# Performance work log

Measured on AMD Instinct MI355X. Metric: run time of the kernel, lower is better.

Reference implementation:

```python
import jax, jax.numpy as jnp
from jax import lax
import numpy as np

WINDOW_SIZE = 11
SIGMA = 1.5
C1 = 0.01 ** 2
C2 = 0.03 ** 2


def _make_window(window_size, channel):
    x = np.arange(window_size) - window_size // 2
    g = np.exp(-(x ** 2) / (2.0 * SIGMA ** 2))
    g = g / g.sum()
    w3 = g[:, None, None] * g[None, :, None] * g[None, None, :]  # [k,k,k]
    w = np.broadcast_to(w3, (channel, 1, window_size, window_size, window_size))
    return jnp.asarray(w.copy(), dtype=jnp.float32)


def setup_inputs() -> dict:
    key = jax.random.key(0)
    k1, k2 = jax.random.split(key)
    shape = (4, 1, 160, 160, 160)
    img1 = jax.random.uniform(k1, shape, dtype=jnp.float32)
    img2 = jax.random.uniform(k2, shape, dtype=jnp.float32)
    window = _make_window(WINDOW_SIZE, shape[1])
    return {"img1": img1, "img2": img2, "window": window}


def _depthwise_conv3d(x, window):
    c = window.shape[0]
    k = window.shape[-1]
    pad = k // 2
    return lax.conv_general_dilated(
        x, window,
        window_strides=(1, 1, 1),
        padding=[(pad, pad)] * 3,
        dimension_numbers=("NCDHW", "OIDHW", "NCDHW"),
        feature_group_count=c,
    )


def reference(img1, img2, window):
    b = img1.shape[0]
    # One conv call over all five window statistics (stacked along batch).
    stacked = jnp.concatenate(
        [img1, img2, img1 * img1, img2 * img2, img1 * img2], axis=0)
    conv = _depthwise_conv3d(stacked, window)
    mu1, mu2, e11, e22, e12 = (conv[i * b:(i + 1) * b] for i in range(5))
    mu1_sq = mu1 * mu1
    mu2_sq = mu2 * mu2
    mu1_mu2 = mu1 * mu2
    sigma1_sq = e11 - mu1_sq
    sigma2_sq = e22 - mu2_sq
    sigma12 = e12 - mu1_mu2
    ssim_map = ((2 * mu1_mu2 + C1) * (2 * sigma12 + C2)) / (
        (mu1_sq + mu2_sq + C1) * (sigma1_sq + sigma2_sq + C2))
    return ssim_map.mean()  # size_average=True
```

## Files before the change

kernel.cpp:

```cpp
#include <hip/hip_runtime.h>
#include <math.h>
#include <type_traits>

typedef float f2 __attribute__((ext_vector_type(2)));
typedef float f4 __attribute__((ext_vector_type(4)));

#define DD 160
#define HH 160
#define WW 160
#define BB 4
#define KK 11
#define RAD 5
#define TH 16
#define TW 16
#define DCH 32
#define NPLANES (DCH + 2 * RAD)
#define NDCH (DD / DCH)
#define HALO_H (TH + 2 * RAD)
#define TS 16
#define STAT (HALO_H * TS)

struct GaussP { float gg[32]; };

__global__ __launch_bounds__(128, 2)
void ssim3d_kernel(const float* __restrict__ img1,
                   const float* __restrict__ img2,
                   float* __restrict__ out, GaussP gp)
{
    __shared__ float tmpA[5 * STAT];
    __shared__ float tmpB[5 * STAT];
    __shared__ float wsum[2];

    const int tid = threadIdx.x;
    const int xc = tid & 7;
    const int ty = tid >> 3;
    const int p1r = tid >> 2;
    const int p1q = tid & 3;

    const int blk = blockIdx.x;
    const int bw = blk % 10;
    const int bh = (blk / 10) % 10;
    const int bd = (blk / 100) % NDCH;
    const int bb = blk / (100 * NDCH);

    const int oh0 = bh * TH, ow0 = bw * TW, od0 = bd * DCH;
    const float* base1 = img1 + (size_t)bb * DD * HH * WW;
    const float* base2 = img2 + (size_t)bb * DD * HH * WW;

    f2 a1[KK], a2[KK], a11[KK], a22[KK], a12[KK];
#pragma unroll
    for (int i = 0; i < KK; ++i) { a1[i]=0.f; a2[i]=0.f; a11[i]=0.f; a22[i]=0.f; a12[i]=0.f; }

    f2 lsum = 0.f;

    const int gh = oh0 - RAD + p1r;
    const bool p1act = (p1r < HALO_H);
    const bool rowok = p1act && ((unsigned)gh < (unsigned)HH);
    const int gc0 = ow0 + 4 * p1q - 8;
    const size_t rowoff = (size_t)((unsigned)gh < (unsigned)HH ? gh : 0) * WW;

    f4 pa[5], pb[5];
#pragma unroll
    for (int j = 0; j < 5; ++j) { pa[j] = (f4)0.f; pb[j] = (f4)0.f; }

    float* twr = tmpA;
    float* trd = tmpB;

    {
        const int dn = od0 - RAD;
        if (p1act && (unsigned)dn < (unsigned)DD) {
            const size_t pbv = (size_t)dn * (HH * WW) + rowoff;
#pragma unroll
            for (int j = 0; j < 5; ++j) {
                const int gc = gc0 + 4 * j;
                f4 za = (f4)0.f, zb = (f4)0.f;
                if (rowok && gc >= 0 && gc <= WW - 4) {
                    za = *(const f4*)(base1 + pbv + gc);
                    zb = *(const f4*)(base2 + pbv + gc);
                }
                pa[j] = za; pb[j] = zb;
            }
        }
    }

    int pcbase = 0;
    auto body = [&](auto uc) {
        constexpr int U = decltype(uc)::value;
        const int p = pcbase + U;
        const int d = od0 - RAD + p;
        const bool dval = (p < NPLANES) && ((unsigned)d < (unsigned)DD);

        if (dval && p1act) {
            f2 q0[5], q1[5];
#pragma unroll
            for (int st = 0; st < 5; ++st) { q0[st] = 0.f; q1[st] = 0.f; }
#pragma unroll
            for (int j = 0; j < 5; ++j) {
#pragma unroll
                for (int ii = 0; ii < 4; ++ii) {
                    const int i = 4 * j + ii;
                    if (i < 3 || i > 16) continue;
                    const float av = pa[j][ii], bv = pb[j][ii];
                    const float aa = av * av, bb2 = bv * bv, ab = av * bv;
                    const f2 w01 = { gp.gg[2*(i-1)], gp.gg[2*(i-1)+1] };
                    const f2 w23 = { gp.gg[2*(i-3)], gp.gg[2*(i-3)+1] };
                    q0[0] += w01 * av;   q1[0] += w23 * av;
                    q0[1] += w01 * bv;   q1[1] += w23 * bv;
                    q0[2] += w01 * aa;   q1[2] += w23 * aa;
                    q0[3] += w01 * bb2;  q1[3] += w23 * bb2;
                    q0[4] += w01 * ab;   q1[4] += w23 * ab;
                }
            }
            float* tw = twr + p1r * TS + 4 * p1q;
#pragma unroll
            for (int st = 0; st < 5; ++st) {
                f4 v;
                v[0] = q0[st][0]; v[1] = q0[st][1];
                v[2] = q1[st][0]; v[3] = q1[st][1];
                *(f4*)(tw + st * STAT) = v;
            }
        }

        {
            const int pn = p + 1;
            const int dn = od0 - RAD + pn;
            if (p1act && (pn < NPLANES) && ((unsigned)dn < (unsigned)DD)) {
                const size_t pbv = (size_t)dn * (HH * WW) + rowoff;
#pragma unroll
                for (int j = 0; j < 5; ++j) {
                    const int gc = gc0 + 4 * j;
                    f4 za = (f4)0.f, zb = (f4)0.f;
                    if (rowok && gc >= 0 && gc <= WW - 4) {
                        za = *(const f4*)(base1 + pbv + gc);
                        zb = *(const f4*)(base2 + pbv + gc);
                    }
                    pa[j] = za; pb[j] = zb;
                }
            }
        }

        if (dval) {
            asm volatile("s_waitcnt lgkmcnt(0)\n\ts_barrier" ::: "memory");
            f2 P1 = 0.f, P2 = 0.f, P11 = 0.f, P22 = 0.f, P12 = 0.f;
            const float* tb = twr + (ty * TS + 2 * xc);
#pragma unroll
            for (int k = 0; k < KK; ++k) {
                const float w = gp.gg[2 * (k + 2)];
                const int o = k * TS;
                P1  += w * *(const f2*)(tb + 0*STAT + o);
                P2  += w * *(const f2*)(tb + 1*STAT + o);
                P11 += w * *(const f2*)(tb + 2*STAT + o);
                P22 += w * *(const f2*)(tb + 3*STAT + o);
                P12 += w * *(const f2*)(tb + 4*STAT + o);
            }
#pragma unroll
            for (int t = 0; t < KK; ++t) {
                constexpr int base = U + 22;
                const int s = (base - t) % 11;
                const float w = gp.gg[2 * (t + 2)];
                a1[s]  += w * P1;
                a2[s]  += w * P2;
                a11[s] += w * P11;
                a22[s] += w * P22;
                a12[s] += w * P12;
            }
        }

        constexpr int e = (U + 1) % 11;
        if (p >= 2 * RAD && p < NPLANES) {
            f2 mu1 = a1[e], mu2 = a2[e];
            f2 m11 = mu1 * mu1, m22 = mu2 * mu2, m12 = mu1 * mu2;
            f2 sg1 = a11[e] - m11, sg2 = a22[e] - m22, sg12 = a12[e] - m12;
            const float C1c = 0.0001f, C2c = 0.0009f;
            f2 num = (2.f * m12 + C1c) * (2.f * sg12 + C2c);
            f2 den = (m11 + m22 + C1c) * (sg1 + sg2 + C2c);
            lsum += num / den;
        }
        a1[e] = 0.f; a2[e] = 0.f; a11[e] = 0.f; a22[e] = 0.f; a12[e] = 0.f;

        float* t = twr; twr = trd; trd = t;
    };

    for (pcbase = 0; pcbase < 44; pcbase += 11) {
        body(std::integral_constant<int, 0>{});
        body(std::integral_constant<int, 1>{});
        body(std::integral_constant<int, 2>{});
        body(std::integral_constant<int, 3>{});
        body(std::integral_constant<int, 4>{});
        body(std::integral_constant<int, 5>{});
        body(std::integral_constant<int, 6>{});
        body(std::integral_constant<int, 7>{});
        body(std::integral_constant<int, 8>{});
        body(std::integral_constant<int, 9>{});
        body(std::integral_constant<int, 10>{});
    }

    float v = lsum.x + lsum.y;
#pragma unroll
    for (int off = 32; off > 0; off >>= 1)
        v += __shfl_down(v, off, 64);
    if ((tid & 63) == 0) wsum[tid >> 6] = v;
    __syncthreads();
    if (tid == 0) {
        const float inv_n = 1.0f / ((float)BB * DD * HH * WW);
        atomicAdd(out, (wsum[0] + wsum[1]) * inv_n);
    }
}

extern "C" void kernel_launch(void* const* d_in, const int* in_sizes, int n_in,
                              void* d_out, int out_size, void* d_ws, size_t ws_size,
                              hipStream_t stream) {
    const float* img1 = (const float*)d_in[0];
    const float* img2 = (const float*)d_in[1];
    float* out = (float*)d_out;

    double gd[KK], sum = 0.0;
    for (int i = 0; i < KK; ++i) {
        double x = (double)(i - KK / 2);
        gd[i] = exp(-(x * x) / (2.0 * 1.5 * 1.5));
        sum += gd[i];
    }
    float gf[KK];
    for (int i = 0; i < KK; ++i) gf[i] = (float)(gd[i] / sum);

    GaussP gp;
    for (int x = 0; x < 16; ++x) {
        const int j0 = x - 2, j1 = x - 3;
        gp.gg[2 * x]     = (j0 >= 0 && j0 < KK) ? gf[j0] : 0.0f;
        gp.gg[2 * x + 1] = (j1 >= 0 && j1 < KK) ? gf[j1] : 0.0f;
    }

    hipMemsetAsync(d_out, 0, sizeof(float), stream);

    dim3 grid(10 * 10 * NDCH * BB);
    dim3 block(128);
    hipLaunchKernelGGL(ssim3d_kernel, grid, block, 0, stream,
                       img1, img2, out, gp);
}
```

Before: 336.3 us.

## Process two depth planes per barrier with quad-buffered shared staging

The depth loop now handles two planes per iteration, staging both planes' horizontally filtered statistics into a four-slot shared buffer so only one barrier is needed per pair of planes. Two register prefetch sets keep two planes of global loads in flight. Phase-1 tasks are remapped so each wavefront uses 52 of its 64 lanes instead of leaving the last wave mostly idle. This halves barrier count and deepens the load pipeline, at the cost of more shared memory and more registers, which may hurt occupancy at two blocks per CU.

New measurement: 454.5 us. 35.2% more time.

```diff
diff --git a/kernel.cpp b/kernel.cpp
--- a/kernel.cpp
+++ b/kernel.cpp
@@ -22,20 +22,24 @@
 
 struct GaussP { float gg[32]; };
 
+template <int N> using ic = std::integral_constant<int, N>;
+
 __global__ __launch_bounds__(128, 2)
 void ssim3d_kernel(const float* __restrict__ img1,
                    const float* __restrict__ img2,
                    float* __restrict__ out, GaussP gp)
 {
-    __shared__ float tmpA[5 * STAT];
-    __shared__ float tmpB[5 * STAT];
+    __shared__ float tmp[4][5 * STAT];
     __shared__ float wsum[2];
 
     const int tid = threadIdx.x;
     const int xc = tid & 7;
     const int ty = tid >> 3;
-    const int p1r = tid >> 2;
-    const int p1q = tid & 3;
+    const int lane = tid & 63;
+    const int task = lane + (tid >> 6) * 52;
+    const bool p1act = lane < 52;
+    const int p1r = task >> 2;
+    const int p1q = task & 3;
 
     const int blk = blockIdx.x;
     const int bw = blk % 10;
@@ -54,21 +58,17 @@
     f2 lsum = 0.f;
 
     const int gh = oh0 - RAD + p1r;
-    const bool p1act = (p1r < HALO_H);
     const bool rowok = p1act && ((unsigned)gh < (unsigned)HH);
     const int gc0 = ow0 + 4 * p1q - 8;
     const size_t rowoff = (size_t)((unsigned)gh < (unsigned)HH ? gh : 0) * WW;
 
-    f4 pa[5], pb[5];
-#pragma unroll
-    for (int j = 0; j < 5; ++j) { pa[j] = (f4)0.f; pb[j] = (f4)0.f; }
-
-    float* twr = tmpA;
-    float* trd = tmpB;
-
-    {
-        const int dn = od0 - RAD;
-        if (p1act && (unsigned)dn < (unsigned)DD) {
+    f4 paA[5], pbA[5], paB[5], pbB[5];
+#pragma unroll
+    for (int j = 0; j < 5; ++j) { paA[j]=(f4)0.f; pbA[j]=(f4)0.f; paB[j]=(f4)0.f; pbB[j]=(f4)0.f; }
+
+    auto prefetch = [&](f4* pa, f4* pb, int pn) {
+        const int dn = od0 - RAD + pn;
+        if (p1act && (pn < NPLANES) && ((unsigned)dn < (unsigned)DD)) {
             const size_t pbv = (size_t)dn * (HH * WW) + rowoff;
 #pragma unroll
             for (int j = 0; j < 5; ++j) {
@@ -81,92 +81,70 @@
                 pa[j] = za; pb[j] = zb;
             }
         }
-    }
-
-    int pcbase = 0;
-    auto body = [&](auto uc) {
-        constexpr int U = decltype(uc)::value;
-        const int p = pcbase + U;
-        const int d = od0 - RAD + p;
-        const bool dval = (p < NPLANES) && ((unsigned)d < (unsigned)DD);
-
-        if (dval && p1act) {
-            f2 q0[5], q1[5];
-#pragma unroll
-            for (int st = 0; st < 5; ++st) { q0[st] = 0.f; q1[st] = 0.f; }
-#pragma unroll
-            for (int j = 0; j < 5; ++j) {
-#pragma unroll
-                for (int ii = 0; ii < 4; ++ii) {
-                    const int i = 4 * j + ii;
-                    if (i < 3 || i > 16) continue;
-                    const float av = pa[j][ii], bv = pb[j][ii];
-                    const float aa = av * av, bb2 = bv * bv, ab = av * bv;
-                    const f2 w01 = { gp.gg[2*(i-1)], gp.gg[2*(i-1)+1] };
-                    const f2 w23 = { gp.gg[2*(i-3)], gp.gg[2*(i-3)+1] };
-                    q0[0] += w01 * av;   q1[0] += w23 * av;
-                    q0[1] += w01 * bv;   q1[1] += w23 * bv;
-                    q0[2] += w01 * aa;   q1[2] += w23 * aa;
-                    q0[3] += w01 * bb2;  q1[3] += w23 * bb2;
-                    q0[4] += w01 * ab;   q1[4] += w23 * ab;
-                }
+    };
+
+    auto phase1 = [&](const f4* pa, const f4* pb, int p) {
+        if (!p1act) return;
+        f2 q0[5], q1[5];
+#pragma unroll
+        for (int st = 0; st < 5; ++st) { q0[st] = 0.f; q1[st] = 0.f; }
+#pragma unroll
+        for (int j = 0; j < 5; ++j) {
+#pragma unroll
+            for (int ii = 0; ii < 4; ++ii) {
+                const int i = 4 * j + ii;
+                if (i < 3 || i > 16) continue;
+                const float av = pa[j][ii], bv = pb[j][ii];
+                const float aa = av * av, bb2 = bv * bv, ab = av * bv;
+                const f2 w01 = { gp.gg[2*(i-1)], gp.gg[2*(i-1)+1] };
+                const f2 w23 = { gp.gg[2*(i-3)], gp.gg[2*(i-3)+1] };
+                q0[0] += w01 * av;   q1[0] += w23 * av;
+                q0[1] += w01 * bv;   q1[1] += w23 * bv;
+                q0[2] += w01 * aa;   q1[2] += w23 * aa;
+                q0[3] += w01 * bb2;  q1[3] += w23 * bb2;
+                q0[4] += w01 * ab;   q1[4] += w23 * ab;
             }
-            float* tw = twr + p1r * TS + 4 * p1q;
-#pragma unroll
-            for (int st = 0; st < 5; ++st) {
-                f4 v;
-                v[0] = q0[st][0]; v[1] = q0[st][1];
-                v[2] = q1[st][0]; v[3] = q1[st][1];
-                *(f4*)(tw + st * STAT) = v;
-            }
-        }
-
-        {
-            const int pn = p + 1;
-            const int dn = od0 - RAD + pn;
-            if (p1act && (pn < NPLANES) && ((unsigned)dn < (unsigned)DD)) {
-                const size_t pbv = (size_t)dn * (HH * WW) + rowoff;
-#pragma unroll
-                for (int j = 0; j < 5; ++j) {
-                    const int gc = gc0 + 4 * j;
-                    f4 za = (f4)0.f, zb = (f4)0.f;
-                    if (rowok && gc >= 0 && gc <= WW - 4) {
-                        za = *(const f4*)(base1 + pbv + gc);
-                        zb = *(const f4*)(base2 + pbv + gc);
-                    }
-                    pa[j] = za; pb[j] = zb;
-                }
-            }
-        }
-
-        if (dval) {
-            asm volatile("s_waitcnt lgkmcnt(0)\n\ts_barrier" ::: "memory");
-            f2 P1 = 0.f, P2 = 0.f, P11 = 0.f, P22 = 0.f, P12 = 0.f;
-            const float* tb = twr + (ty * TS + 2 * xc);
-#pragma unroll
-            for (int k = 0; k < KK; ++k) {
-                const float w = gp.gg[2 * (k + 2)];
-                const int o = k * TS;
-                P1  += w * *(const f2*)(tb + 0*STAT + o);
-                P2  += w * *(const f2*)(tb + 1*STAT + o);
-                P11 += w * *(const f2*)(tb + 2*STAT + o);
-                P22 += w * *(const f2*)(tb + 3*STAT + o);
-                P12 += w * *(const f2*)(tb + 4*STAT + o);
-            }
-#pragma unroll
-            for (int t = 0; t < KK; ++t) {
-                constexpr int base = U + 22;
-                const int s = (base - t) % 11;
-                const float w = gp.gg[2 * (t + 2)];
-                a1[s]  += w * P1;
-                a2[s]  += w * P2;
-                a11[s] += w * P11;
-                a22[s] += w * P22;
-                a12[s] += w * P12;
-            }
-        }
-
-        constexpr int e = (U + 1) % 11;
+        }
+        float* tw = tmp[p & 3] + p1r * TS + 4 * p1q;
+#pragma unroll
+        for (int st = 0; st < 5; ++st) {
+            f4 v;
+            v[0] = q0[st][0]; v[1] = q0[st][1];
+            v[2] = q1[st][0]; v[3] = q1[st][1];
+            *(f4*)(tw + st * STAT) = v;
+        }
+    };
+
+    auto phase2 = [&](auto ucU, int p) {
+        constexpr int UU = decltype(ucU)::value;
+        f2 P1 = 0.f, P2 = 0.f, P11 = 0.f, P22 = 0.f, P12 = 0.f;
+        const float* tb = tmp[p & 3] + (ty * TS + 2 * xc);
+#pragma unroll
+        for (int k = 0; k < KK; ++k) {
+            const float w = gp.gg[2 * (k + 2)];
+            const int o = k * TS;
+            P1  += w * *(const f2*)(tb + 0*STAT + o);
+            P2  += w * *(const f2*)(tb + 1*STAT + o);
+            P11 += w * *(const f2*)(tb + 2*STAT + o);
+            P22 += w * *(const f2*)(tb + 3*STAT + o);
+            P12 += w * *(const f2*)(tb + 4*STAT + o);
+        }
+#pragma unroll
+        for (int t = 0; t < KK; ++t) {
+            constexpr int base = UU + 22;
+            const int s = (base - t) % 11;
+            const float w = gp.gg[2 * (t + 2)];
+            a1[s]  += w * P1;
+            a2[s]  += w * P2;
+            a11[s] += w * P11;
+            a22[s] += w * P22;
+            a12[s] += w * P12;
+        }
+    };
+
+    auto emitp = [&](auto ucU, int p) {
+        constexpr int UU = decltype(ucU)::value;
+        constexpr int e = (UU + 1) % 11;
         if (p >= 2 * RAD && p < NPLANES) {
             f2 mu1 = a1[e], mu2 = a2[e];
             f2 m11 = mu1 * mu1, m22 = mu2 * mu2, m12 = mu1 * mu2;
@@ -177,22 +155,47 @@
             lsum += num / den;
         }
         a1[e] = 0.f; a2[e] = 0.f; a11[e] = 0.f; a22[e] = 0.f; a12[e] = 0.f;
-
-        float* t = twr; twr = trd; trd = t;
-    };
-
-    for (pcbase = 0; pcbase < 44; pcbase += 11) {
-        body(std::integral_constant<int, 0>{});
-        body(std::integral_constant<int, 1>{});
-        body(std::integral_constant<int, 2>{});
-        body(std::integral_constant<int, 3>{});
-        body(std::integral_constant<int, 4>{});
-        body(std::integral_constant<int, 5>{});
-        body(std::integral_constant<int, 6>{});
-        body(std::integral_constant<int, 7>{});
-        body(std::integral_constant<int, 8>{});
-        body(std::integral_constant<int, 9>{});
-        body(std::integral_constant<int, 10>{});
+    };
+
+    prefetch(paA, pbA, 0);
+    prefetch(paB, pbB, 1);
+
+    int pcbase = 0;
+    auto iter = [&](auto ucv) {
+        constexpr int V = decltype(ucv)::value;
+        const int p0 = pcbase + 2 * V;
+        const int p1 = p0 + 1;
+        const int d0 = od0 - RAD + p0;
+        const bool dval0 = (p0 < NPLANES) && ((unsigned)d0 < (unsigned)DD);
+        const bool dval1 = (p1 < NPLANES) && ((unsigned)(d0 + 1) < (unsigned)DD);
+
+        if (dval0) phase1(paA, pbA, p0);
+        prefetch(paA, pbA, p0 + 2);
+        if (dval1) phase1(paB, pbB, p1);
+        prefetch(paB, pbB, p1 + 2);
+
+        if (dval0 || dval1) {
+            asm volatile("s_waitcnt lgkmcnt(0)\n\ts_barrier" ::: "memory");
+        }
+
+        if (dval0) phase2(ic<(2 * V) % 11>{}, p0);
+        emitp(ic<(2 * V) % 11>{}, p0);
+        if (dval1) phase2(ic<(2 * V + 1) % 11>{}, p1);
+        emitp(ic<(2 * V + 1) % 11>{}, p1);
+    };
+
+    for (pcbase = 0; pcbase < 44; pcbase += 22) {
+        iter(ic<0>{});
+        iter(ic<1>{});
+        iter(ic<2>{});
+        iter(ic<3>{});
+        iter(ic<4>{});
+        iter(ic<5>{});
+        iter(ic<6>{});
+        iter(ic<7>{});
+        iter(ic<8>{});
+        iter(ic<9>{});
+        iter(ic<10>{});
     }
 
     float v = lsum.x + lsum.y;
```

## Shrink tile to one wavefront per block and drop the LDS barrier

Applied to the files above, without the earlier changes.

Halves the tile width so each block is a single 64-thread wavefront, doubles the grid, and replaces the s_barrier with just an lgkmcnt wait. The shared-memory stride is padded from 16 to 20, and the cross-wave final reduction is removed. The aim is to remove workgroup barrier stalls and gain scheduling flexibility. In exchange, the relative halo overhead in W grows (8-wide outputs need 18 input columns), so each output costs more global loads and more first-pass convolution work.

Measured after the change: 437.9 us. 1.3x slower.

```diff
diff --git a/kernel.cpp b/kernel.cpp
--- a/kernel.cpp
+++ b/kernel.cpp
@@ -12,36 +12,37 @@
 #define KK 11
 #define RAD 5
 #define TH 16
-#define TW 16
+#define TW 8
 #define DCH 32
 #define NPLANES (DCH + 2 * RAD)
 #define NDCH (DD / DCH)
 #define HALO_H (TH + 2 * RAD)
-#define TS 16
+#define TS 20
 #define STAT (HALO_H * TS)
 
 struct GaussP { float gg[32]; };
 
-__global__ __launch_bounds__(128, 2)
+template <int N> using ic = std::integral_constant<int, N>;
+
+__global__ __launch_bounds__(64, 2)
 void ssim3d_kernel(const float* __restrict__ img1,
                    const float* __restrict__ img2,
                    float* __restrict__ out, GaussP gp)
 {
-    __shared__ float tmpA[5 * STAT];
-    __shared__ float tmpB[5 * STAT];
-    __shared__ float wsum[2];
+    __shared__ float tmp[2][5 * STAT];
 
     const int tid = threadIdx.x;
-    const int xc = tid & 7;
-    const int ty = tid >> 3;
-    const int p1r = tid >> 2;
-    const int p1q = tid & 3;
+    const int xc = tid & 3;
+    const int ty = tid >> 2;
+    const int p1r = tid >> 1;
+    const int p1q = tid & 1;
+    const bool p1act = tid < 52;
 
     const int blk = blockIdx.x;
-    const int bw = blk % 10;
-    const int bh = (blk / 10) % 10;
-    const int bd = (blk / 100) % NDCH;
-    const int bb = blk / (100 * NDCH);
+    const int bw = blk % 20;
+    const int bh = (blk / 20) % 10;
+    const int bd = (blk / 200) % NDCH;
+    const int bb = blk / 1000;
 
     const int oh0 = bh * TH, ow0 = bw * TW, od0 = bd * DCH;
     const float* base1 = img1 + (size_t)bb * DD * HH * WW;
@@ -54,7 +55,6 @@
     f2 lsum = 0.f;
 
     const int gh = oh0 - RAD + p1r;
-    const bool p1act = (p1r < HALO_H);
     const bool rowok = p1act && ((unsigned)gh < (unsigned)HH);
     const int gc0 = ow0 + 4 * p1q - 8;
     const size_t rowoff = (size_t)((unsigned)gh < (unsigned)HH ? gh : 0) * WW;
@@ -63,12 +63,9 @@
 #pragma unroll
     for (int j = 0; j < 5; ++j) { pa[j] = (f4)0.f; pb[j] = (f4)0.f; }
 
-    float* twr = tmpA;
-    float* trd = tmpB;
-
-    {
-        const int dn = od0 - RAD;
-        if (p1act && (unsigned)dn < (unsigned)DD) {
+    auto prefetch = [&](int pn) {
+        const int dn = od0 - RAD + pn;
+        if (p1act && (pn < NPLANES) && ((unsigned)dn < (unsigned)DD)) {
             const size_t pbv = (size_t)dn * (HH * WW) + rowoff;
 #pragma unroll
             for (int j = 0; j < 5; ++j) {
@@ -81,7 +78,9 @@
                 pa[j] = za; pb[j] = zb;
             }
         }
-    }
+    };
+
+    prefetch(0);
 
     int pcbase = 0;
     auto body = [&](auto uc) {
@@ -111,7 +110,7 @@
                     q0[4] += w01 * ab;   q1[4] += w23 * ab;
                 }
             }
-            float* tw = twr + p1r * TS + 4 * p1q;
+            float* tw = tmp[p & 1] + p1r * TS + 4 * p1q;
 #pragma unroll
             for (int st = 0; st < 5; ++st) {
                 f4 v;
@@ -121,28 +120,12 @@
             }
         }
 
-        {
-            const int pn = p + 1;
-            const int dn = od0 - RAD + pn;
-            if (p1act && (pn < NPLANES) && ((unsigned)dn < (unsigned)DD)) {
-                const size_t pbv = (size_t)dn * (HH * WW) + rowoff;
-#pragma unroll
-                for (int j = 0; j < 5; ++j) {
-                    const int gc = gc0 + 4 * j;
-                    f4 za = (f4)0.f, zb = (f4)0.f;
-                    if (rowok && gc >= 0 && gc <= WW - 4) {
-                        za = *(const f4*)(base1 + pbv + gc);
-                        zb = *(const f4*)(base2 + pbv + gc);
-                    }
-                    pa[j] = za; pb[j] = zb;
-                }
-            }
-        }
+        prefetch(p + 1);
 
         if (dval) {
-            asm volatile("s_waitcnt lgkmcnt(0)\n\ts_barrier" ::: "memory");
+            asm volatile("s_waitcnt lgkmcnt(0)" ::: "memory");
             f2 P1 = 0.f, P2 = 0.f, P11 = 0.f, P22 = 0.f, P12 = 0.f;
-            const float* tb = twr + (ty * TS + 2 * xc);
+            const float* tb = tmp[p & 1] + (ty * TS + 2 * xc);
 #pragma unroll
             for (int k = 0; k < KK; ++k) {
                 const float w = gp.gg[2 * (k + 2)];
@@ -177,33 +160,29 @@
             lsum += num / den;
         }
         a1[e] = 0.f; a2[e] = 0.f; a11[e] = 0.f; a22[e] = 0.f; a12[e] = 0.f;
-
-        float* t = twr; twr = trd; trd = t;
     };
 
     for (pcbase = 0; pcbase < 44; pcbase += 11) {
-        body(std::integral_constant<int, 0>{});
-        body(std::integral_constant<int, 1>{});
-        body(std::integral_constant<int, 2>{});
-        body(std::integral_constant<int, 3>{});
-        body(std::integral_constant<int, 4>{});
-        body(std::integral_constant<int, 5>{});
-        body(std::integral_constant<int, 6>{});
-        body(std::integral_constant<int, 7>{});
-        body(std::integral_constant<int, 8>{});
-        body(std::integral_constant<int, 9>{});
-        body(std::integral_constant<int, 10>{});
+        body(ic<0>{});
+        body(ic<1>{});
+        body(ic<2>{});
+        body(ic<3>{});
+        body(ic<4>{});
+        body(ic<5>{});
+        body(ic<6>{});
+        body(ic<7>{});
+        body(ic<8>{});
+        body(ic<9>{});
+        body(ic<10>{});
     }
 
     float v = lsum.x + lsum.y;
 #pragma unroll
     for (int off = 32; off > 0; off >>= 1)
         v += __shfl_down(v, off, 64);
-    if ((tid & 63) == 0) wsum[tid >> 6] = v;
-    __syncthreads();
     if (tid == 0) {
         const float inv_n = 1.0f / ((float)BB * DD * HH * WW);
-        atomicAdd(out, (wsum[0] + wsum[1]) * inv_n);
+        atomicAdd(out, v * inv_n);
     }
 }
 
@@ -232,8 +211,8 @@
 
     hipMemsetAsync(d_out, 0, sizeof(float), stream);
 
-    dim3 grid(10 * 10 * NDCH * BB);
-    dim3 block(128);
+    dim3 grid(20 * 10 * NDCH * BB);
+    dim3 block(64);
     hipLaunchKernelGGL(ssim3d_kernel, grid, block, 0, stream,
                        img1, img2, out, gp);
 }
```
